# Performance work log

Measured on AMD Instinct MI355X. Metric: run time of the kernel, lower is better.

The kernel has to match this reference:

```python
import jax, jax.numpy as jnp
import numpy as np

NEG = -10000000000.0  # matches the torch module's additive mask value


def _span_attn(enc, logit_tok, starts, ends, qb, bsz):
    # enc: [bsz, seq, d]; logit_tok: [bsz, seq]; starts/ends/qb: [Q]
    seq = enc.shape[1]
    pos = jnp.arange(seq)
    # span mask: token t belongs to span iff start <= t <= end (inclusive)
    mask = (pos[None, :] >= starts[:, None]) & (pos[None, :] <= ends[:, None])  # [Q, seq]
    logits = logit_tok[qb] + (1.0 - mask.astype(enc.dtype)) * NEG               # [Q, seq]
    w = jax.nn.softmax(logits, axis=1)                                           # [Q, seq]
    # avoid materializing enc[qb] ([Q, seq, d]): contract against every batch row,
    # then select the right batch with a one-hot (p is tiny: [Q, bsz, d]).
    p = jnp.einsum('qs,bsd->qbd', w, enc)
    oh = jax.nn.one_hot(qb, bsz, dtype=enc.dtype)
    return jnp.einsum('qbd,qb->qd', p, oh)


def setup_inputs() -> dict:
    key = jax.random.key(0)
    ks = jax.random.split(key, 10)
    bsz, seq, hd, pd, Q = 8, 2048, 1024, 256, 8192
    enc = jax.random.normal(ks[0], (bsz, seq, hd), dtype=jnp.float32)
    proj_w = jax.random.normal(ks[1], (hd, pd), dtype=jnp.float32) * (1.0 / np.sqrt(hd))
    proj_b = jnp.zeros((pd,), dtype=jnp.float32)
    attn_w = jax.random.normal(ks[2], (pd,), dtype=jnp.float32) * (1.0 / np.sqrt(pd))
    attn_b = jnp.zeros((), dtype=jnp.float32)

    def make_spans(k):
        k1, k2, k3 = jax.random.split(k, 3)
        s = jax.random.randint(k1, (Q,), 0, seq)
        ln = jax.random.randint(k2, (Q,), 0, 32)
        e = jnp.minimum(s + ln, seq - 1)
        return s, e

    s1, e1 = make_spans(ks[3])
    s2, e2 = make_spans(ks[4])
    qb = jax.random.randint(ks[5], (Q,), 0, bsz)
    return {
        'flag': 0,
        'encoded_input': enc,
        'start_ids_1': s1,
        'end_ids_1': e1,
        'query_batch_idx': qb,
        'start_ids_2': s2,
        'end_ids_2': e2,
        'proj_w': proj_w,
        'proj_b': proj_b,
        'attn_w': attn_w,
        'attn_b': attn_b,
    }


def reference(flag, encoded_input, start_ids_1, end_ids_1, query_batch_idx,
              start_ids_2, end_ids_2, proj_w, proj_b, attn_w, attn_b):
    del flag  # unused in the original forward
    bsz = encoded_input.shape[0]
    enc = encoded_input @ proj_w + proj_b                 # use_proj=True path
    logit_tok = jnp.einsum('bsd,d->bs', enc, attn_w) + attn_b  # Linear(d,1)
    res1 = _span_attn(enc, logit_tok, start_ids_1, end_ids_1, query_batch_idx, bsz)
    res2 = _span_attn(enc, logit_tok, start_ids_2, end_ids_2, query_batch_idx, bsz)
    return (res1, res2)
```

## Files before the change

### kernel.cpp

```cpp
#include <hip/hip_runtime.h>

typedef __attribute__((ext_vector_type(8))) short bf16x8;
typedef __attribute__((ext_vector_type(4))) float f32x4;

#define LDK 40

__device__ __forceinline__ float bf2f(unsigned short u) {
    union { unsigned int i; float f; } v; v.i = ((unsigned int)u) << 16; return v.f;
}
__device__ __forceinline__ unsigned short f2bf(float f) {
    union { float f; unsigned int i; } v; v.f = f;
    unsigned int x = v.i;
    return (unsigned short)((x + 0x7FFFu + ((x >> 16) & 1u)) >> 16);
}

__device__ __forceinline__ void gload16(const void* g, void* l) {
    __builtin_amdgcn_global_load_lds(
        (const __attribute__((address_space(1))) unsigned int*)g,
        (__attribute__((address_space(3))) unsigned int*)l, 16, 0, 0);
}

#define ASM_LGKM0 { asm volatile("s_waitcnt lgkmcnt(0)" ::: "memory"); \
                    __builtin_amdgcn_sched_barrier(0); }
#define ASM_BAR   asm volatile("s_barrier" ::: "memory")

__global__ __launch_bounds__(256) void transpose_b_kernel(
    const float* __restrict__ B, unsigned short* __restrict__ Bt, int K, int N)
{
    __shared__ float tile[32][33];
    int kb = blockIdx.x % (K / 32);
    int nb = blockIdx.x / (K / 32);
    int k0 = kb * 32, n0 = nb * 32;
    int tx = threadIdx.x & 31, ty = threadIdx.x >> 5;
    #pragma unroll
    for (int i = 0; i < 4; ++i)
        tile[ty + 8 * i][tx] = B[(size_t)(k0 + ty + 8 * i) * N + n0 + tx];
    __syncthreads();
    #pragma unroll
    for (int i = 0; i < 4; ++i)
        Bt[(size_t)(n0 + ty + 8 * i) * K + k0 + tx] = f2bf(tile[tx][ty + 8 * i]);
}

__global__ __launch_bounds__(256, 4) void gemm_mfma_kernel(
    const float* __restrict__ A, const unsigned short* __restrict__ Bt,
    const float* __restrict__ bias, const float* __restrict__ attn_w,
    unsigned short* __restrict__ C, float* __restrict__ logit,
    int M, int N, int K)
{
    __shared__ __attribute__((aligned(16))) unsigned short AsA[2][64 * LDK];
    __shared__ __attribute__((aligned(16))) unsigned short AsB[2][64 * 32];

    const int tid = threadIdx.x;
    const int bid = blockIdx.x;
    const int xcd = bid & 7;
    const int j   = bid >> 3;
    const int bn  = (j & 3) * 64;
    const int bm  = (xcd * 32 + (j >> 2)) * 64;

    const int lane = tid & 63;
    const int wave = tid >> 6;
    const int wr = (wave >> 1) * 32;
    const int wc = (wave & 1) * 32;

    const int srow = tid >> 2;
    const int sk   = (tid & 3) * 8;
    const float* Aptr = A + (size_t)(bm + srow) * K + sk;

    const int brow = 16 * wave + (lane >> 2);
    const int bsl  = (lane & 3) ^ ((lane >> 3) & 3);
    const unsigned short* Bptr = Bt + (size_t)(bn + brow) * K + bsl * 8;
    unsigned short* ldsB0 = &AsB[0][wave * 512];
    unsigned short* ldsB1 = &AsB[1][wave * 512];

    float4 areg[2][2];
    f32x4 acc[2][2];
    #pragma unroll
    for (int m = 0; m < 2; ++m)
        #pragma unroll
        for (int n = 0; n < 2; ++n)
            acc[m][n] = (f32x4){0.f, 0.f, 0.f, 0.f};

    const int c15 = lane & 15;
    const int g4  = lane >> 4;
    const int kg8 = g4 * 8;
    const int slB = (g4 ^ ((c15 >> 1) & 3)) * 8;

    const int nk = K / 32;

    gload16(Bptr, ldsB0);
    areg[0][0] = *(const float4*)(Aptr);
    areg[0][1] = *(const float4*)(Aptr + 4);
    asm volatile("s_waitcnt vmcnt(0)" ::: "memory");
    {
        unsigned short tmp[8];
        const float* afp = (const float*)areg[0];
        #pragma unroll
        for (int i = 0; i < 8; ++i) tmp[i] = f2bf(afp[i]);
        *(bf16x8*)&AsA[0][srow * LDK + sk] = *(bf16x8*)&tmp[0];
    }
    gload16(Bptr + 32, ldsB1);
    areg[1][0] = *(const float4*)(Aptr + 32);
    areg[1][1] = *(const float4*)(Aptr + 36);
    ASM_LGKM0;
    ASM_BAR;

#define BODY(T, S)                                                            \
    {                                                                         \
        bf16x8 af0 = *(bf16x8*)&AsA[S][(wr + c15) * LDK + kg8];               \
        bf16x8 af1 = *(bf16x8*)&AsA[S][(wr + 16 + c15) * LDK + kg8];          \
        bf16x8 bf0 = *(bf16x8*)&AsB[S][(wc + c15) * 32 + slB];                \
        bf16x8 bf1 = *(bf16x8*)&AsB[S][(wc + 16 + c15) * 32 + slB];           \
        ASM_LGKM0;                                                            \
        ASM_BAR;                            \
        if ((T) + 2 < nk) {                                                   \
            gload16(Bptr + ((T) + 2) * 32, (S) ? ldsB1 : ldsB0);              \
            areg[S][0] = *(const float4*)(Aptr + ((T) + 2) * 32);             \
            areg[S][1] = *(const float4*)(Aptr + ((T) + 2) * 32 + 4);         \
        }                                                                     \
        __builtin_amdgcn_s_setprio(1);                                        \
        acc[0][0] = __builtin_amdgcn_mfma_f32_16x16x32_bf16(af0, bf0, acc[0][0], 0, 0, 0); \
        acc[0][1] = __builtin_amdgcn_mfma_f32_16x16x32_bf16(af0, bf1, acc[0][1], 0, 0, 0); \
        acc[1][0] = __builtin_amdgcn_mfma_f32_16x16x32_bf16(af1, bf0, acc[1][0], 0, 0, 0); \
        acc[1][1] = __builtin_amdgcn_mfma_f32_16x16x32_bf16(af1, bf1, acc[1][1], 0, 0, 0); \
        __builtin_amdgcn_s_setprio(0);                                        \
        if ((T) + 1 < nk) {                                                   \
            if ((T) + 2 < nk) { asm volatile("s_waitcnt vmcnt(3)" ::: "memory"); } \
            else              { asm volatile("s_waitcnt vmcnt(0)" ::: "memory"); } \
            unsigned short tmp[8];                                            \
            const float* afp = (const float*)areg[1 - (S)];                   \
            _Pragma("unroll")                                                 \
            for (int i = 0; i < 8; ++i) tmp[i] = f2bf(afp[i]);                \
            *(bf16x8*)&AsA[1 - (S)][srow * LDK + sk] = *(bf16x8*)&tmp[0];     \
            ASM_LGKM0;                                                        \
        }                                                                     \
        ASM_BAR;                                           \
    }

    for (int t = 0; t < nk; t += 2) {
        BODY(t, 0)
        BODY(t + 1, 1)
    }
#undef BODY

    const int col0 = bn + wc + c15;
    const int row0 = bm + wr + g4 * 4;
    float wsum[2][4] = {};
    #pragma unroll
    for (int n = 0; n < 2; ++n) {
        float bv  = bias[col0 + n * 16];
        float awv = attn_w[col0 + n * 16];
        #pragma unroll
        for (int m = 0; m < 2; ++m) {
            #pragma unroll
            for (int i = 0; i < 4; ++i) {
                float cf = acc[m][n][i] + bv;
                C[(size_t)(row0 + m * 16 + i) * N + col0 + n * 16] = f2bf(cf);
                wsum[m][i] += cf * awv;
            }
        }
    }
    #pragma unroll
    for (int m = 0; m < 2; ++m) {
        #pragma unroll
        for (int i = 0; i < 4; ++i) {
            float v = wsum[m][i];
            v += __shfl_xor(v, 1, 64);
            v += __shfl_xor(v, 2, 64);
            v += __shfl_xor(v, 4, 64);
            v += __shfl_xor(v, 8, 64);
            if (c15 == 0) atomicAdd(&logit[row0 + m * 16 + i], v);
        }
    }
}

__global__ __launch_bounds__(256) void span_kernel(
    const unsigned short* __restrict__ enc, const float* __restrict__ logit,
    const int* __restrict__ s1, const int* __restrict__ e1,
    const int* __restrict__ s2, const int* __restrict__ e2,
    const int* __restrict__ qb, float* __restrict__ out,
    int Q, int seq, int pd)
{
    int lane = threadIdx.x & 63;
    int q = blockIdx.x * 4 + (threadIdx.x >> 6);
    int r  = (q >= Q) ? 1 : 0;
    int qi = q - r * Q;
    int s = r ? s2[qi] : s1[qi];
    int e = r ? e2[qi] : e1[qi];
    int b = qb[qi];
    int len = e - s + 1;

    const float* lp = logit + (size_t)b * seq + s;
    float lg = (lane < len) ? lp[lane] : -3.4e38f;
    float m = lg;
    #pragma unroll
    for (int off = 32; off; off >>= 1) m = fmaxf(m, __shfl_xor(m, off, 64));
    float p = (lane < len) ? __expf(lg - m) : 0.0f;
    float sum = p;
    #pragma unroll
    for (int off = 32; off; off >>= 1) sum += __shfl_xor(sum, off, 64);
    float inv = 1.0f / sum;

    const unsigned short* ep = enc + ((size_t)b * seq + s) * pd + lane * 4;
    float ax = 0.f, ay = 0.f, az = 0.f, aw = 0.f;

    for (int t0 = 0; t0 < len; t0 += 16) {
        ushort4 ev[16];
        #pragma unroll
        for (int u = 0; u < 16; ++u) {
            int tc = t0 + u;
            tc = (tc < len) ? tc : (len - 1);
            ev[u] = *(const ushort4*)(ep + (size_t)tc * pd);
        }
        #pragma unroll
        for (int u = 0; u < 16; ++u) {
            float wt = __shfl(p, t0 + u, 64);
            ax += wt * bf2f(ev[u].x);
            ay += wt * bf2f(ev[u].y);
            az += wt * bf2f(ev[u].z);
            aw += wt * bf2f(ev[u].w);
        }
    }
    float4 res = {ax * inv, ay * inv, az * inv, aw * inv};
    *((float4*)(out + (size_t)q * pd) + lane) = res;
}

extern "C" void kernel_launch(void* const* d_in, const int* in_sizes, int n_in,
                              void* d_out, int out_size, void* d_ws, size_t ws_size,
                              hipStream_t stream) {
    const float* enc_in = (const float*)d_in[1];
    const int*   s1     = (const int*)d_in[2];
    const int*   e1     = (const int*)d_in[3];
    const int*   qb     = (const int*)d_in[4];
    const int*   s2     = (const int*)d_in[5];
    const int*   e2     = (const int*)d_in[6];
    const float* proj_w = (const float*)d_in[7];
    const float* proj_b = (const float*)d_in[8];
    const float* attn_w = (const float*)d_in[9];
    float* out = (float*)d_out;

    const int Q   = in_sizes[2];
    const int pd  = in_sizes[8];
    const int hd  = in_sizes[7] / pd;
    const int seq = 2048;
    const int M   = in_sizes[1] / hd;

    unsigned short* enc_bf = (unsigned short*)d_ws;
    float*          logit  = (float*)((char*)d_ws + (size_t)M * pd * 2);
    unsigned short* Btw    = (unsigned short*)((char*)d_ws +
                               (size_t)M * pd * 2 + (size_t)M * 4);

    hipMemsetAsync(logit, 0, (size_t)M * sizeof(float), stream);
    transpose_b_kernel<<<(hd / 32) * (pd / 32), 256, 0, stream>>>(proj_w, Btw, hd, pd);
    gemm_mfma_kernel<<<(M / 64) * (pd / 64), 256, 0, stream>>>(
        enc_in, Btw, proj_b, attn_w, enc_bf, logit, M, pd, hd);
    span_kernel<<<2 * Q / 4, 256, 0, stream>>>(
        enc_bf, logit, s1, e1, s2, e2, qb, out, Q, seq, pd);
}
```

Before: 172.7 us.

## Shrink GEMM tile to 64x32 and sort span queries by batch and position

The projection GEMM now uses a 64x32 output tile with one MFMA row per wave and a simpler single-stage double-buffered loop with __syncthreads. It also drops the custom waitcnt and priority tricks and allows up to eight blocks per CU. Separately, new histogram, scan and scatter kernels bucket span queries by (batch, start/64) so the span kernel visits queries in locality order and reuses cached rows of the encoded tensor. This adds three small kernel launches and a memset, and the GEMM reads each A tile twice as often because N is split across more blocks.

Measured after the change: 208.8 us. +20.9%, slower.

```diff
diff --git a/kernel.cpp b/kernel.cpp
--- a/kernel.cpp
+++ b/kernel.cpp
@@ -13,16 +13,11 @@
     unsigned int x = v.i;
     return (unsigned short)((x + 0x7FFFu + ((x >> 16) & 1u)) >> 16);
 }
-
 __device__ __forceinline__ void gload16(const void* g, void* l) {
     __builtin_amdgcn_global_load_lds(
         (const __attribute__((address_space(1))) unsigned int*)g,
         (__attribute__((address_space(3))) unsigned int*)l, 16, 0, 0);
 }
-
-#define ASM_LGKM0 { asm volatile("s_waitcnt lgkmcnt(0)" ::: "memory"); \
-                    __builtin_amdgcn_sched_barrier(0); }
-#define ASM_BAR   asm volatile("s_barrier" ::: "memory")
 
 __global__ __launch_bounds__(256) void transpose_b_kernel(
     const float* __restrict__ B, unsigned short* __restrict__ Bt, int K, int N)
@@ -41,147 +36,162 @@
         Bt[(size_t)(n0 + ty + 8 * i) * K + k0 + tx] = f2bf(tile[tx][ty + 8 * i]);
 }
 
-__global__ __launch_bounds__(256, 4) void gemm_mfma_kernel(
+__global__ __launch_bounds__(256, 8) void gemm_mfma_kernel(
     const float* __restrict__ A, const unsigned short* __restrict__ Bt,
     const float* __restrict__ bias, const float* __restrict__ attn_w,
     unsigned short* __restrict__ C, float* __restrict__ logit,
     int M, int N, int K)
 {
     __shared__ __attribute__((aligned(16))) unsigned short AsA[2][64 * LDK];
-    __shared__ __attribute__((aligned(16))) unsigned short AsB[2][64 * 32];
+    __shared__ __attribute__((aligned(16))) unsigned short AsB[2][32 * 32];
 
     const int tid = threadIdx.x;
     const int bid = blockIdx.x;
     const int xcd = bid & 7;
     const int j   = bid >> 3;
-    const int bn  = (j & 3) * 64;
-    const int bm  = (xcd * 32 + (j >> 2)) * 64;
+    const int bn  = (j & 7) * 32;
+    const int bm  = (xcd * 32 + (j >> 3)) * 64;
 
     const int lane = tid & 63;
     const int wave = tid >> 6;
-    const int wr = (wave >> 1) * 32;
-    const int wc = (wave & 1) * 32;
-
-    const int srow = tid >> 2;
-    const int sk   = (tid & 3) * 8;
-    const float* Aptr = A + (size_t)(bm + srow) * K + sk;
-
-    const int brow = 16 * wave + (lane >> 2);
-    const int bsl  = (lane & 3) ^ ((lane >> 3) & 3);
-    const unsigned short* Bptr = Bt + (size_t)(bn + brow) * K + bsl * 8;
-    unsigned short* ldsB0 = &AsB[0][wave * 512];
-    unsigned short* ldsB1 = &AsB[1][wave * 512];
-
-    float4 areg[2][2];
-    f32x4 acc[2][2];
-    #pragma unroll
-    for (int m = 0; m < 2; ++m)
-        #pragma unroll
-        for (int n = 0; n < 2; ++n)
-            acc[m][n] = (f32x4){0.f, 0.f, 0.f, 0.f};
-
-    const int c15 = lane & 15;
-    const int g4  = lane >> 4;
-    const int kg8 = g4 * 8;
-    const int slB = (g4 ^ ((c15 >> 1) & 3)) * 8;
+    const int c15  = lane & 15;
+    const int g4   = lane >> 4;
+    const int kg8  = g4 * 8;
+    const int slB  = (g4 ^ ((c15 >> 1) & 3)) * 8;
+
+    const int arow = tid >> 2;
+    const int akq  = (tid & 3) * 8;
+    const float* Aptr = A + (size_t)(bm + arow) * K + akq;
+
+    const int brow  = (tid & 127) >> 2;
+    const int bslot = (tid & 3) ^ ((tid >> 3) & 3);
+    const unsigned short* Bptr = Bt + (size_t)(bn + brow) * K + bslot * 8;
+
+    f32x4 acc[2];
+    acc[0] = (f32x4){0.f, 0.f, 0.f, 0.f};
+    acc[1] = (f32x4){0.f, 0.f, 0.f, 0.f};
 
     const int nk = K / 32;
 
-    gload16(Bptr, ldsB0);
-    areg[0][0] = *(const float4*)(Aptr);
-    areg[0][1] = *(const float4*)(Aptr + 4);
-    asm volatile("s_waitcnt vmcnt(0)" ::: "memory");
+    if (tid < 128) gload16(Bptr, &AsB[0][(tid >> 6) * 512]);
     {
+        float4 a0 = *(const float4*)(Aptr);
+        float4 a1 = *(const float4*)(Aptr + 4);
         unsigned short tmp[8];
-        const float* afp = (const float*)areg[0];
-        #pragma unroll
-        for (int i = 0; i < 8; ++i) tmp[i] = f2bf(afp[i]);
-        *(bf16x8*)&AsA[0][srow * LDK + sk] = *(bf16x8*)&tmp[0];
-    }
-    gload16(Bptr + 32, ldsB1);
-    areg[1][0] = *(const float4*)(Aptr + 32);
-    areg[1][1] = *(const float4*)(Aptr + 36);
-    ASM_LGKM0;
-    ASM_BAR;
-
-#define BODY(T, S)                                                            \
-    {                                                                         \
-        bf16x8 af0 = *(bf16x8*)&AsA[S][(wr + c15) * LDK + kg8];               \
-        bf16x8 af1 = *(bf16x8*)&AsA[S][(wr + 16 + c15) * LDK + kg8];          \
-        bf16x8 bf0 = *(bf16x8*)&AsB[S][(wc + c15) * 32 + slB];                \
-        bf16x8 bf1 = *(bf16x8*)&AsB[S][(wc + 16 + c15) * 32 + slB];           \
-        ASM_LGKM0;                                                            \
-        ASM_BAR;                            \
-        if ((T) + 2 < nk) {                                                   \
-            gload16(Bptr + ((T) + 2) * 32, (S) ? ldsB1 : ldsB0);              \
-            areg[S][0] = *(const float4*)(Aptr + ((T) + 2) * 32);             \
-            areg[S][1] = *(const float4*)(Aptr + ((T) + 2) * 32 + 4);         \
-        }                                                                     \
-        __builtin_amdgcn_s_setprio(1);                                        \
-        acc[0][0] = __builtin_amdgcn_mfma_f32_16x16x32_bf16(af0, bf0, acc[0][0], 0, 0, 0); \
-        acc[0][1] = __builtin_amdgcn_mfma_f32_16x16x32_bf16(af0, bf1, acc[0][1], 0, 0, 0); \
-        acc[1][0] = __builtin_amdgcn_mfma_f32_16x16x32_bf16(af1, bf0, acc[1][0], 0, 0, 0); \
-        acc[1][1] = __builtin_amdgcn_mfma_f32_16x16x32_bf16(af1, bf1, acc[1][1], 0, 0, 0); \
-        __builtin_amdgcn_s_setprio(0);                                        \
-        if ((T) + 1 < nk) {                                                   \
-            if ((T) + 2 < nk) { asm volatile("s_waitcnt vmcnt(3)" ::: "memory"); } \
-            else              { asm volatile("s_waitcnt vmcnt(0)" ::: "memory"); } \
-            unsigned short tmp[8];                                            \
-            const float* afp = (const float*)areg[1 - (S)];                   \
-            _Pragma("unroll")                                                 \
-            for (int i = 0; i < 8; ++i) tmp[i] = f2bf(afp[i]);                \
-            *(bf16x8*)&AsA[1 - (S)][srow * LDK + sk] = *(bf16x8*)&tmp[0];     \
-            ASM_LGKM0;                                                        \
-        }                                                                     \
-        ASM_BAR;                                           \
-    }
-
-    for (int t = 0; t < nk; t += 2) {
-        BODY(t, 0)
-        BODY(t + 1, 1)
-    }
-#undef BODY
-
-    const int col0 = bn + wc + c15;
-    const int row0 = bm + wr + g4 * 4;
-    float wsum[2][4] = {};
+        const float* af = (const float*)&a0;
+        #pragma unroll
+        for (int i = 0; i < 4; ++i) tmp[i] = f2bf(af[i]);
+        af = (const float*)&a1;
+        #pragma unroll
+        for (int i = 0; i < 4; ++i) tmp[4 + i] = f2bf(af[i]);
+        *(bf16x8*)&AsA[0][arow * LDK + akq] = *(bf16x8*)&tmp[0];
+    }
+    __syncthreads();
+
+    for (int t = 0; t < nk; ++t) {
+        const int s = t & 1;
+        float4 a0n, a1n;
+        const bool more = (t + 1 < nk);
+        if (more) {
+            if (tid < 128) gload16(Bptr + (t + 1) * 32, &AsB[1 - s][(tid >> 6) * 512]);
+            a0n = *(const float4*)(Aptr + (t + 1) * 32);
+            a1n = *(const float4*)(Aptr + (t + 1) * 32 + 4);
+        }
+        bf16x8 af  = *(bf16x8*)&AsA[s][(wave * 16 + c15) * LDK + kg8];
+        bf16x8 bf0 = *(bf16x8*)&AsB[s][c15 * 32 + slB];
+        bf16x8 bf1 = *(bf16x8*)&AsB[s][(16 + c15) * 32 + slB];
+        acc[0] = __builtin_amdgcn_mfma_f32_16x16x32_bf16(af, bf0, acc[0], 0, 0, 0);
+        acc[1] = __builtin_amdgcn_mfma_f32_16x16x32_bf16(af, bf1, acc[1], 0, 0, 0);
+        if (more) {
+            unsigned short tmp[8];
+            const float* afp = (const float*)&a0n;
+            #pragma unroll
+            for (int i = 0; i < 4; ++i) tmp[i] = f2bf(afp[i]);
+            afp = (const float*)&a1n;
+            #pragma unroll
+            for (int i = 0; i < 4; ++i) tmp[4 + i] = f2bf(afp[i]);
+            *(bf16x8*)&AsA[1 - s][arow * LDK + akq] = *(bf16x8*)&tmp[0];
+        }
+        __syncthreads();
+    }
+
+    const int col0 = bn + c15;
+    const int row0 = bm + wave * 16 + g4 * 4;
+    float wsum[4] = {};
     #pragma unroll
     for (int n = 0; n < 2; ++n) {
         float bv  = bias[col0 + n * 16];
         float awv = attn_w[col0 + n * 16];
         #pragma unroll
-        for (int m = 0; m < 2; ++m) {
-            #pragma unroll
-            for (int i = 0; i < 4; ++i) {
-                float cf = acc[m][n][i] + bv;
-                C[(size_t)(row0 + m * 16 + i) * N + col0 + n * 16] = f2bf(cf);
-                wsum[m][i] += cf * awv;
-            }
-        }
-    }
-    #pragma unroll
-    for (int m = 0; m < 2; ++m) {
-        #pragma unroll
         for (int i = 0; i < 4; ++i) {
-            float v = wsum[m][i];
-            v += __shfl_xor(v, 1, 64);
-            v += __shfl_xor(v, 2, 64);
-            v += __shfl_xor(v, 4, 64);
-            v += __shfl_xor(v, 8, 64);
-            if (c15 == 0) atomicAdd(&logit[row0 + m * 16 + i], v);
-        }
-    }
+            float cf = acc[n][i] + bv;
+            C[(size_t)(row0 + i) * N + col0 + n * 16] = f2bf(cf);
+            wsum[i] += cf * awv;
+        }
+    }
+    #pragma unroll
+    for (int i = 0; i < 4; ++i) {
+        float v = wsum[i];
+        v += __shfl_xor(v, 1, 64);
+        v += __shfl_xor(v, 2, 64);
+        v += __shfl_xor(v, 4, 64);
+        v += __shfl_xor(v, 8, 64);
+        if (c15 == 0) atomicAdd(&logit[row0 + i], v);
+    }
+}
+
+__global__ __launch_bounds__(256) void hist_kernel(
+    const int* __restrict__ s1, const int* __restrict__ s2,
+    const int* __restrict__ qb, int* __restrict__ cnt, int Q)
+{
+    int j = blockIdx.x * 256 + threadIdx.x;
+    if (j >= 2 * Q) return;
+    int qi = (j < Q) ? j : j - Q;
+    int s  = (j < Q) ? s1[qi] : s2[qi];
+    atomicAdd(&cnt[qb[qi] * 32 + (s >> 6)], 1);
+}
+
+__global__ __launch_bounds__(256) void scan_kernel(
+    const int* __restrict__ cnt, int* __restrict__ off)
+{
+    __shared__ int tmp[256];
+    int tid = threadIdx.x;
+    int v = cnt[tid];
+    tmp[tid] = v;
+    __syncthreads();
+    #pragma unroll
+    for (int d = 1; d < 256; d <<= 1) {
+        int x = (tid >= d) ? tmp[tid - d] : 0;
+        __syncthreads();
+        tmp[tid] += x;
+        __syncthreads();
+    }
+    off[tid] = tmp[tid] - v;
+}
+
+__global__ __launch_bounds__(256) void scatter_kernel(
+    const int* __restrict__ s1, const int* __restrict__ s2,
+    const int* __restrict__ qb, int* __restrict__ off,
+    int* __restrict__ perm, int Q)
+{
+    int j = blockIdx.x * 256 + threadIdx.x;
+    if (j >= 2 * Q) return;
+    int qi = (j < Q) ? j : j - Q;
+    int s  = (j < Q) ? s1[qi] : s2[qi];
+    int pos = atomicAdd(&off[qb[qi] * 32 + (s >> 6)], 1);
+    perm[pos] = j;
 }
 
 __global__ __launch_bounds__(256) void span_kernel(
     const unsigned short* __restrict__ enc, const float* __restrict__ logit,
     const int* __restrict__ s1, const int* __restrict__ e1,
     const int* __restrict__ s2, const int* __restrict__ e2,
-    const int* __restrict__ qb, float* __restrict__ out,
-    int Q, int seq, int pd)
+    const int* __restrict__ qb, const int* __restrict__ perm,
+    float* __restrict__ out, int Q, int seq, int pd)
 {
     int lane = threadIdx.x & 63;
-    int q = blockIdx.x * 4 + (threadIdx.x >> 6);
+    int gid = blockIdx.x * 4 + (threadIdx.x >> 6);
+    int q = perm[gid];
     int r  = (q >= Q) ? 1 : 0;
     int qi = q - r * Q;
     int s = r ? s2[qi] : s1[qi];
@@ -244,15 +254,24 @@
     const int seq = 2048;
     const int M   = in_sizes[1] / hd;
 
-    unsigned short* enc_bf = (unsigned short*)d_ws;
-    float*          logit  = (float*)((char*)d_ws + (size_t)M * pd * 2);
-    unsigned short* Btw    = (unsigned short*)((char*)d_ws +
-                               (size_t)M * pd * 2 + (size_t)M * 4);
+    char* ws = (char*)d_ws;
+    unsigned short* enc_bf = (unsigned short*)ws;            ws += (size_t)M * pd * 2;
+    float*          logit  = (float*)ws;                     ws += (size_t)M * 4;
+    unsigned short* Btw    = (unsigned short*)ws;            ws += (size_t)pd * hd * 2;
+    int*            cnt    = (int*)ws;                       ws += 256 * 4;
+    int*            off    = (int*)ws;                       ws += 256 * 4;
+    int*            perm   = (int*)ws;                       ws += (size_t)2 * Q * 4;
 
     hipMemsetAsync(logit, 0, (size_t)M * sizeof(float), stream);
+    hipMemsetAsync(cnt, 0, 256 * sizeof(int), stream);
+
+    hist_kernel<<<(2 * Q + 255) / 256, 256, 0, stream>>>(s1, s2, qb, cnt, Q);
+    scan_kernel<<<1, 256, 0, stream>>>(cnt, off);
+    scatter_kernel<<<(2 * Q + 255) / 256, 256, 0, stream>>>(s1, s2, qb, off, perm, Q);
+
     transpose_b_kernel<<<(hd / 32) * (pd / 32), 256, 0, stream>>>(proj_w, Btw, hd, pd);
-    gemm_mfma_kernel<<<(M / 64) * (pd / 64), 256, 0, stream>>>(
+    gemm_mfma_kernel<<<(M / 64) * (pd / 32), 256, 0, stream>>>(
         enc_in, Btw, proj_b, attn_w, enc_bf, logit, M, pd, hd);
     span_kernel<<<2 * Q / 4, 256, 0, stream>>>(
-        enc_bf, logit, s1, e1, s2, e2, qb, out, Q, seq, pd);
-}
+        enc_bf, logit, s1, e1, s2, e2, qb, perm, out, Q, seq, pd);
+}
```
